# Kernel tuning notes

Measured on AMD Instinct MI355X. Metric: run time of the kernel, lower is better.

Reference implementation:

```python
import jax, jax.numpy as jnp
import numpy as np

KT = 0.5
KG = 0.5

def _ln(x, g, b, eps=1e-5):
    m = x.mean(-1, keepdims=True)
    v = ((x - m) ** 2).mean(-1, keepdims=True)
    return (x - m) / jnp.sqrt(v + eps) * g + b

def _sin_pe(pos, d):
    # pos: [...] float positions -> [..., d] sinusoidal encoding
    half = d // 2
    div = jnp.exp(jnp.arange(half, dtype=jnp.float32) * jnp.float32(-np.log(10000.0) * 2.0 / d))
    ang = pos[..., None].astype(jnp.float32) * div
    return jnp.concatenate([jnp.sin(ang), jnp.cos(ang)], axis=-1)

def _geo_encode(idx, emb_qk_w, w1, b1, w2, b2, ln1_g, ln1_b, ln2_g, ln2_b):
    gd = emb_qk_w.shape[-1]
    Lg = idx.shape[-1]
    x = emb_qk_w[idx]                                   # (B, S, Lg, gd)
    x = x + _sin_pe(jnp.arange(Lg, dtype=jnp.float32), gd)
    scale = 1.0 / np.sqrt(gd)
    for i in range(w1.shape[0]):
        s = jnp.einsum('bsqd,bskd->bsqk', x, x) * scale
        a = jax.nn.softmax(s, axis=-1)
        c = jnp.einsum('bsqk,bskd->bsqd', a, x)
        x = _ln(x + c, ln1_g[i], ln1_b[i])
        h = jax.nn.relu(x @ w1[i] + b1[i]) @ w2[i] + b2[i]
        x = _ln(x + h, ln2_g[i], ln2_b[i])
    return x.mean(-2)                                   # (B, S, gd)

def _forward(src_poi, src_quadkey, padding_mask, attn_mask, tgt_poi, tgt_quadkey,
             key_padding_mask, mem_mask, data_size,
             src_time, tm, gm, emb_poi_w, emb_qk_w,
             geo_ffn_w1, geo_ffn_b1, geo_ffn_w2, geo_ffn_b2,
             geo_ln1_g, geo_ln1_b, geo_ln2_g, geo_ln2_b,
             enc_wq, enc_wk, enc_wv, enc_ffn_w1, enc_ffn_b1, enc_ffn_w2, enc_ffn_b2,
             enc_ln1_g, enc_ln1_b, enc_ln2_g, enc_ln2_b,
             dec_wq, dec_wk, dec_wv, dec_ln_g, dec_ln_b, norm_g, norm_b):
    NEG = jnp.float32(-1e9)
    L = src_poi.shape[1]
    D = norm_g.shape[0]
    geo = lambda idx: _geo_encode(idx, emb_qk_w, geo_ffn_w1, geo_ffn_b1, geo_ffn_w2,
                                  geo_ffn_b2, geo_ln1_g, geo_ln1_b, geo_ln2_g, geo_ln2_b)
    src = jnp.concatenate([emb_poi_w[src_poi], geo(src_quadkey)], axis=-1)   # (B, L, D)
    tgt = jnp.concatenate([emb_poi_w[tgt_poi], geo(tgt_quadkey)], axis=-1)   # (B, Lt, D)
    # time-aware positional encoding: continuous positions from normalized timestamps
    t0 = src_time[:, :1]; tN = src_time[:, -1:]
    pos = (src_time - t0) / (tN - t0 + 1e-9) * (L - 1)
    src = src + _sin_pe(pos, D)
    # relation matrix: threshold intervals at kt/kg, then per-batch max-inversion (vectorizes the per-i loop)
    tmc = jnp.minimum(tm, KT)
    gmc = jnp.minimum(gm, KG)
    tmc = tmc.max(axis=(1, 2), keepdims=True) - tmc
    gmc = gmc.max(axis=(1, 2), keepdims=True) - gmc
    rel = tmc + gmc                                     # (B, L, L)
    scale = 1.0 / np.sqrt(D)
    emask = attn_mask[None, :, :] | padding_mask[:, None, :]
    for i in range(enc_wq.shape[0]):                    # Interval Aware Attention Blocks
        q = src @ enc_wq[i]; k = src @ enc_wk[i]; v = src @ enc_wv[i]
        s = jnp.einsum('bqd,bkd->bqk', q, k) * scale + rel
        a = jax.nn.softmax(jnp.where(emask, NEG, s), axis=-1)
        c = jnp.einsum('bqk,bkd->bqd', a, v)
        src = _ln(src + c, enc_ln1_g[i], enc_ln1_b[i])
        h = jax.nn.relu(src @ enc_ffn_w1[i] + enc_ffn_b1[i]) @ enc_ffn_w2[i] + enc_ffn_b2[i]
        src = _ln(src + h, enc_ln2_g[i], enc_ln2_b[i])
    # target-aware decoder (eval path: last encoder state broadcast over candidates)
    mem = jnp.broadcast_to(src[:, -1:, :], tgt.shape)
    dmask = mem_mask[None, :, :] | key_padding_mask[:, None, :]
    x = tgt
    for i in range(dec_wq.shape[0]):
        q = x @ dec_wq[i]; k = mem @ dec_wk[i]; v = mem @ dec_wv[i]
        s = jnp.einsum('bqd,bkd->bqk', q, k) * scale
        a = jax.nn.softmax(jnp.where(dmask, NEG, s), axis=-1)
        c = jnp.einsum('bqk,bkd->bqd', a, v)
        x = _ln(x + c, dec_ln_g[i], dec_ln_b[i])
    out = _ln(x + mem, norm_g, norm_b)
    return jnp.sum(out * tgt, axis=-1)                  # (B, Lt) matching scores

def setup_inputs():
    key = jax.random.key(0)
    ks = iter(jax.random.split(key, 64))
    nk = lambda: next(ks)
    B, L, Lg, Lt = 512, 100, 12, 101
    n_poi, n_qk = 100000, 4096
    ed, gd = 192, 64
    D = ed + gd
    Ng, Ni, Nd = 2, 2, 1
    p = lambda *s: (jax.random.normal(nk(), s, jnp.float32) * 0.02)
    return {
        'src_poi': jax.random.randint(nk(), (B, L), 0, n_poi),
        'src_quadkey': jax.random.randint(nk(), (B, L, Lg), 0, n_qk),
        'src_time': jnp.sort(jax.random.uniform(nk(), (B, L), jnp.float32) * 1e4, axis=-1),
        'tm': jax.random.uniform(nk(), (B, L, L), jnp.float32),
        'gm': jax.random.uniform(nk(), (B, L, L), jnp.float32),
        'padding_mask': jnp.zeros((B, L), bool),
        'attn_mask': jnp.triu(jnp.ones((L, L), bool), k=1),
        'tgt_poi': jax.random.randint(nk(), (B, Lt), 0, n_poi),
        'tgt_quadkey': jax.random.randint(nk(), (B, Lt, Lg), 0, n_qk),
        'key_padding_mask': jnp.zeros((B, Lt), bool),
        'mem_mask': jnp.zeros((Lt, Lt), bool),
        'data_size': jnp.full((B,), L, jnp.int32),
        'emb_poi_w': p(n_poi, ed),
        'emb_qk_w': p(n_qk, gd),
        'geo_ffn_w1': p(Ng, gd, 2 * gd), 'geo_ffn_b1': jnp.zeros((Ng, 2 * gd)),
        'geo_ffn_w2': p(Ng, 2 * gd, gd), 'geo_ffn_b2': jnp.zeros((Ng, gd)),
        'geo_ln1_g': jnp.ones((Ng, gd)), 'geo_ln1_b': jnp.zeros((Ng, gd)),
        'geo_ln2_g': jnp.ones((Ng, gd)), 'geo_ln2_b': jnp.zeros((Ng, gd)),
        'enc_wq': p(Ni, D, D), 'enc_wk': p(Ni, D, D), 'enc_wv': p(Ni, D, D),
        'enc_ffn_w1': p(Ni, D, 2 * D), 'enc_ffn_b1': jnp.zeros((Ni, 2 * D)),
        'enc_ffn_w2': p(Ni, 2 * D, D), 'enc_ffn_b2': jnp.zeros((Ni, D)),
        'enc_ln1_g': jnp.ones((Ni, D)), 'enc_ln1_b': jnp.zeros((Ni, D)),
        'enc_ln2_g': jnp.ones((Ni, D)), 'enc_ln2_b': jnp.zeros((Ni, D)),
        'dec_wq': p(Nd, D, D), 'dec_wk': p(Nd, D, D), 'dec_wv': p(Nd, D, D),
        'dec_ln_g': jnp.ones((Nd, D)), 'dec_ln_b': jnp.zeros((Nd, D)),
        'norm_g': jnp.ones((D,)), 'norm_b': jnp.zeros((D,)),
    }

def reference(src_poi, src_quadkey, src_time, tm, gm, padding_mask, attn_mask,
              tgt_poi, tgt_quadkey, key_padding_mask, mem_mask, data_size,
              emb_poi_w, emb_qk_w,
              geo_ffn_w1, geo_ffn_b1, geo_ffn_w2, geo_ffn_b2,
              geo_ln1_g, geo_ln1_b, geo_ln2_g, geo_ln2_b,
              enc_wq, enc_wk, enc_wv, enc_ffn_w1, enc_ffn_b1, enc_ffn_w2, enc_ffn_b2,
              enc_ln1_g, enc_ln1_b, enc_ln2_g, enc_ln2_b,
              dec_wq, dec_wk, dec_wv, dec_ln_g, dec_ln_b, norm_g, norm_b):
    return _forward(src_poi, src_quadkey, padding_mask, attn_mask, tgt_poi, tgt_quadkey,
                    key_padding_mask, mem_mask, data_size,
                    src_time, tm, gm, emb_poi_w, emb_qk_w,
                    geo_ffn_w1, geo_ffn_b1, geo_ffn_w2, geo_ffn_b2,
                    geo_ln1_g, geo_ln1_b, geo_ln2_g, geo_ln2_b,
                    enc_wq, enc_wk, enc_wv, enc_ffn_w1, enc_ffn_b1, enc_ffn_w2, enc_ffn_b2,
                    enc_ln1_g, enc_ln1_b, enc_ln2_g, enc_ln2_b,
                    dec_wq, dec_wk, dec_wv, dec_ln_g, dec_ln_b, norm_g, norm_b)
```

## Files before the change

kernel.cpp:

```cpp
#include <hip/hip_runtime.h>
#include <hip/hip_bf16.h>
#include <stdint.h>

typedef unsigned short u16;
typedef unsigned int   u32;
typedef __attribute__((ext_vector_type(8))) short v8s;
typedef __attribute__((ext_vector_type(4))) float v4f;

__device__ __forceinline__ float b2f(u16 u){ return __uint_as_float(((u32)u) << 16); }
__device__ __forceinline__ float lo2f(u32 u){ return __uint_as_float(u << 16); }
__device__ __forceinline__ float hi2f(u32 u){ return __uint_as_float(u & 0xffff0000u); }
__device__ __forceinline__ u16 f2b(float f){
    __hip_bfloat16 h = __float2bfloat16(f);
    return *reinterpret_cast<u16*>(&h);
}
__device__ __forceinline__ float ldm(const void* p, size_t i, int isbf){
    return isbf ? b2f(((const u16*)p)[i]) : ((const float*)p)[i];
}
__device__ __forceinline__ float wred_sum(float v){
    #pragma unroll
    for (int o = 32; o > 0; o >>= 1) v += __shfl_xor(v, o, 64);
    return v;
}
__device__ __forceinline__ float wred_max(float v){
    #pragma unroll
    for (int o = 32; o > 0; o >>= 1) v = fmaxf(v, __shfl_xor(v, o, 64));
    return v;
}
__device__ __forceinline__ float wred16_sum(float v){
    #pragma unroll
    for (int o = 8; o > 0; o >>= 1) v += __shfl_xor(v, o, 64);
    return v;
}
__device__ __forceinline__ float wred16_max(float v){
    #pragma unroll
    for (int o = 8; o > 0; o >>= 1) v = fmaxf(v, __shfl_xor(v, o, 64));
    return v;
}
__device__ __forceinline__ float block_sum256(float v, float* red, int tid){
    float s = wred_sum(v);
    __syncthreads();
    if ((tid & 63) == 0) red[tid >> 6] = s;
    __syncthreads();
    return red[0] + red[1] + red[2] + red[3];
}
__device__ __forceinline__ void block_sum2(float& a, float& b, float (*red)[2], int tid){
    a = wred_sum(a); b = wred_sum(b);
    __syncthreads();
    if ((tid & 63) == 0){ red[tid >> 6][0] = a; red[tid >> 6][1] = b; }
    __syncthreads();
    a = red[0][0] + red[1][0] + red[2][0] + red[3][0];
    b = red[0][1] + red[1][1] + red[2][1] + red[3][1];
}
__device__ __forceinline__ void lds_fence(){
    asm volatile("s_waitcnt lgkmcnt(0)" ::: "memory");
    __builtin_amdgcn_sched_barrier(0);
}

__global__ void probe_kernel(const u32* __restrict__ ng, int* __restrict__ flag){
    if (threadIdx.x == 0) *flag = (ng[0] == 0x3F803F80u) ? 1 : 0;
}

#define NSEG 25
struct ConvArgs {
    const void* src[NSEG];
    u16*        dst[NSEG];
    int         n[NSEG];
};
__global__ __launch_bounds__(256) void convert_kernel(ConvArgs a, const int* __restrict__ flag){
    int seg = blockIdx.y;
    int i = blockIdx.x * 256 + threadIdx.x;
    if (i >= a.n[seg]) return;
    int isbf = *flag;
    a.dst[seg][i] = f2b(ldm(a.src[seg], i, isbf));
}
__global__ __launch_bounds__(256) void convert_time_kernel(const void* __restrict__ src,
                                                           float* __restrict__ dst,
                                                           const int* __restrict__ flag){
    int i = blockIdx.x * 256 + threadIdx.x;
    if (i >= 51200) return;
    dst[i] = ldm(src, i, *flag);
}

__global__ __launch_bounds__(256) void packfrag_kernel(
    const u16* __restrict__ W, u16* __restrict__ out, int K, int N, int nlayer)
{
    int i = blockIdx.x * 256 + threadIdx.x;
    int total = nlayer * K * N;
    if (i >= total) return;
    int j = i & 7, lane = (i >> 3) & 63, fc = i >> 9;
    int CT = K >> 5, NT = N >> 4;
    int c = fc % CT, nt = (fc / CT) % NT, layer = fc / (CT * NT);
    int k = c * 32 + ((lane >> 4) << 3) + j, n = (nt << 4) + (lane & 15);
    out[i] = W[(layer * K + k) * N + n];
}

__global__ __launch_bounds__(256) void packfrag3_kernel(
    const u16* __restrict__ Wq, const u16* __restrict__ Wk, const u16* __restrict__ Wv,
    u16* __restrict__ out)
{
    int i = blockIdx.x * 256 + threadIdx.x;
    if (i >= 786432) return;
    int j = i & 7, lane = (i >> 3) & 63, fc = i >> 9;
    int c = fc & 7, nt = (fc >> 3) % 48, layer = fc / (8 * 48);
    int k = c * 32 + ((lane >> 4) << 3) + j, n = (nt << 4) + (lane & 15);
    const u16* W = (n < 256) ? Wq : (n < 512) ? Wk : Wv;
    out[i] = W[(layer * 256 + k) * 256 + (n & 255)];
}

template<int ACT, int SPLIT>
__global__ __launch_bounds__(256) void gemm2_kernel(
    const u16* __restrict__ A, const u16* __restrict__ Bf,
    const u16* __restrict__ bias,
    u16* __restrict__ C0, u16* __restrict__ C1, u16* __restrict__ C2,
    int M, int N, int K)
{
    const int tid = threadIdx.x, w = tid >> 6, lane = tid & 63;
    const int wm = w >> 1, wn = w & 1;
    const int m0 = blockIdx.x * 128 + wm * 64;
    const int n0 = blockIdx.y * 128 + wn * 64;
    const int CT = K >> 5;
    const int l15 = lane & 15, lg = lane >> 4;

    v4f acc[4][4];
    #pragma unroll
    for (int mt = 0; mt < 4; mt++)
        #pragma unroll
        for (int nt = 0; nt < 4; nt++) acc[mt][nt] = (v4f){0.f, 0.f, 0.f, 0.f};

    const u16* Arow = A + (size_t)(m0 + l15) * K + (lg << 3);
    const u16* Bbase = Bf + (((size_t)(n0 >> 4) * CT) << 9) + (lane << 3);

    for (int c = 0; c < CT; c++){
        v8s bfr[4];
        #pragma unroll
        for (int nt = 0; nt < 4; nt++)
            bfr[nt] = *(const v8s*)(Bbase + (((size_t)(nt * CT + c)) << 9));
        #pragma unroll
        for (int mt = 0; mt < 4; mt++){
            v8s af = *(const v8s*)(Arow + (size_t)(mt << 4) * K + (c << 5));
            #pragma unroll
            for (int nt = 0; nt < 4; nt++)
                acc[mt][nt] = __builtin_amdgcn_mfma_f32_16x16x32_bf16(af, bfr[nt], acc[mt][nt], 0, 0, 0);
        }
    }

    #pragma unroll
    for (int nt = 0; nt < 4; nt++){
        int colbase = n0 + (nt << 4);
        float bv = bias ? b2f(bias[colbase + l15]) : 0.f;
        u16* Cp; int cw;
        if (SPLIT){
            int nb = colbase >> 8;
            Cp = (nb == 0) ? C0 : (nb == 1) ? C1 : C2;
            cw = 256;
            colbase &= 255;
        } else { Cp = C0; cw = N; }
        #pragma unroll
        for (int mt = 0; mt < 4; mt++)
            #pragma unroll
            for (int r = 0; r < 4; r++){
                int row = m0 + (mt << 4) + (lg << 2) + r;
                float v = acc[mt][nt][r] + bv;
                if (ACT) v = fmaxf(v, 0.f);
                Cp[(size_t)row * cw + colbase + l15] = f2b(v);
            }
    }
}

__global__ __launch_bounds__(256) void gemm3_kernel(
    const u16* __restrict__ A, const u16* __restrict__ Bf,
    const u16* __restrict__ bias, u16* __restrict__ SRC,
    const u16* __restrict__ g, const u16* __restrict__ bta)
{
    __shared__ float red[64][4][2];
    const int tid = threadIdx.x, w = tid >> 6, lane = tid & 63;
    const int l15 = lane & 15, lg = lane >> 4;
    const int m0 = blockIdx.x * 64;
    const int n0 = w * 64;
    const int CT = 16;

    v4f acc[4][4];
    #pragma unroll
    for (int mt = 0; mt < 4; mt++)
        #pragma unroll
        for (int nt = 0; nt < 4; nt++) acc[mt][nt] = (v4f){0.f, 0.f, 0.f, 0.f};

    const u16* Arow = A + (size_t)(m0 + l15) * 512 + (lg << 3);
    const u16* Bbase = Bf + (((size_t)(n0 >> 4) * CT) << 9) + (lane << 3);

    for (int c = 0; c < CT; c++){
        v8s bfr[4];
        #pragma unroll
        for (int nt = 0; nt < 4; nt++)
            bfr[nt] = *(const v8s*)(Bbase + (((size_t)(nt * CT + c)) << 9));
        #pragma unroll
        for (int mt = 0; mt < 4; mt++){
            v8s af = *(const v8s*)(Arow + (size_t)(mt << 4) * 512 + (c << 5));
            #pragma unroll
            for (int nt = 0; nt < 4; nt++)
                acc[mt][nt] = __builtin_amdgcn_mfma_f32_16x16x32_bf16(af, bfr[nt], acc[mt][nt], 0, 0, 0);
        }
    }

    float bv[4];
    #pragma unroll
    for (int nt = 0; nt < 4; nt++) bv[nt] = b2f(bias[n0 + (nt << 4) + l15]);
    #pragma unroll
    for (int mt = 0; mt < 4; mt++){
        #pragma unroll
        for (int r = 0; r < 4; r++){
            int row = m0 + (mt << 4) + (lg << 2) + r;
            float s1 = 0.f, s2 = 0.f;
            #pragma unroll
            for (int nt = 0; nt < 4; nt++){
                int col = n0 + (nt << 4) + l15;
                float y = acc[mt][nt][r] + bv[nt] + b2f(SRC[(size_t)row * 256 + col]);
                acc[mt][nt][r] = y;
                s1 += y; s2 += y * y;
            }
            s1 = wred16_sum(s1); s2 = wred16_sum(s2);
            if (l15 == 0){
                int rr = (mt << 4) + (lg << 2) + r;
                red[rr][w][0] = s1; red[rr][w][1] = s2;
            }
        }
    }
    __syncthreads();
    float gv[4], bb[4];
    #pragma unroll
    for (int nt = 0; nt < 4; nt++){
        gv[nt] = b2f(g[n0 + (nt << 4) + l15]);
        bb[nt] = b2f(bta[n0 + (nt << 4) + l15]);
    }
    #pragma unroll
    for (int mt = 0; mt < 4; mt++){
        #pragma unroll
        for (int r = 0; r < 4; r++){
            int rr = (mt << 4) + (lg << 2) + r;
            int row = m0 + rr;
            float S1 = red[rr][0][0] + red[rr][1][0] + red[rr][2][0] + red[rr][3][0];
            float S2 = red[rr][0][1] + red[rr][1][1] + red[rr][2][1] + red[rr][3][1];
            float mu = S1 * (1.0f / 256.0f);
            float var = S2 * (1.0f / 256.0f) - mu * mu;
            float rs = rsqrtf(var + 1e-5f);
            #pragma unroll
            for (int nt = 0; nt < 4; nt++){
                int col = n0 + (nt << 4) + l15;
                SRC[(size_t)row * 256 + col] = f2b((acc[mt][nt][r] - mu) * rs * gv[nt] + bb[nt]);
            }
        }
    }
}

#define GX1(r,b) (((((r) << 7) | (b))) ^ (((r) & 7) << 4))
#define GH1(r,b) (((((r) << 8) | (b))) ^ (((r) & 7) << 4))

__global__ __launch_bounds__(64) void geo6_kernel(
    const int* __restrict__ src_qk, const int* __restrict__ tgt_qk,
    const u16* __restrict__ emb,
    const u16* __restrict__ w1f, const u16* __restrict__ b1,
    const u16* __restrict__ w2f, const u16* __restrict__ b2,
    const u16* __restrict__ ln1g, const u16* __restrict__ ln1b,
    const u16* __restrict__ ln2g, const u16* __restrict__ ln2b,
    u16* __restrict__ SRC, u16* __restrict__ TGT)
{
    __shared__ __align__(16) u16 xs[16 * 64];
    __shared__ __align__(16) u16 hs[16 * 128];
    __shared__ __align__(16) float Ps[16][20];

    int seq = blockIdx.x;
    const int* qk = src_qk;
    u16* outp = SRC;
    if (seq >= 51200){ qk = tgt_qk; outp = TGT; seq -= 51200; }

    const int lane = threadIdx.x;
    const int g = lane >> 4, m = lane & 15;

    v8s ones;
    #pragma unroll
    for (int j = 0; j < 8; j++) ones[j] = (short)0x3F80;

    {
        float dv = __expf(-(float)(lane & 31) * 0.28782313662425572f);
        const bool issin = lane < 32;
        #pragma unroll
        for (int t = 0; t < 12; t++){
            int idx = qk[seq * 12 + t];
            float ang = (float)t * dv;
            float pe = issin ? __sinf(ang) : __cosf(ang);
            xs[GX1(t, lane << 1) >> 1] = f2b(b2f(emb[idx * 64 + lane]) + pe);
        }
        #pragma unroll
        for (int r = 12; r < 16; r++) xs[GX1(r, lane << 1) >> 1] = (u16)0;
    }
    lds_fence();

    float fsum = 0.f;
    const bool isdiag = (g == (m >> 2)) && (m < 12);
    const int dr = m & 3;

    for (int layer = 0; layer < 2; layer++){
        v4f S = {0.f, 0.f, 0.f, 0.f};
        {
            v8s f0 = *(const v8s*)((const char*)xs + GX1(m, (g << 4)));
            v8s f1 = *(const v8s*)((const char*)xs + GX1(m, 64 + (g << 4)));
            S = __builtin_amdgcn_mfma_f32_16x16x32_bf16(f0, f0, S, 0, 0, 0);
            S = __builtin_amdgcn_mfma_f32_16x16x32_bf16(f1, f1, S, 0, 0, 0);
        }
        {
            float ex[4];
            #pragma unroll
            for (int r = 0; r < 4; r++) ex[r] = (m < 12) ? __expf(S[r] * 0.125f) : 0.f;
            #pragma unroll
            for (int r = 0; r < 4; r++){
                float s = wred16_sum(ex[r]);
                ex[r] = ex[r] / s;
            }
            #pragma unroll
            for (int r = 0; r < 4; r++) Ps[(g << 2) + r][m] = ex[r];
        }
        lds_fence();

        float y[12];
        {
            float xr[12];
            #pragma unroll
            for (int k = 0; k < 12; k++) xr[k] = b2f(xs[GX1(k, lane << 1) >> 1]);
            #pragma unroll
            for (int q = 0; q < 12; q++){
                float4 pa = *(const float4*)&Ps[q][0];
                float4 pb = *(const float4*)&Ps[q][4];
                float4 pc = *(const float4*)&Ps[q][8];
                float c = pa.x*xr[0]+pa.y*xr[1]+pa.z*xr[2]+pa.w*xr[3]
                        + pb.x*xr[4]+pb.y*xr[5]+pb.z*xr[6]+pb.w*xr[7]
                        + pc.x*xr[8]+pc.y*xr[9]+pc.z*xr[10]+pc.w*xr[11];
                y[q] = xr[q] + c;
                xs[GX1(q, lane << 1) >> 1] = f2b(y[q]);
            }
        }
        lds_fence();

        {
            v4f R = {0.f,0.f,0.f,0.f}, Q = {0.f,0.f,0.f,0.f};
            v8s f0 = *(const v8s*)((const char*)xs + GX1(m, (g << 4)));
            v8s f1 = *(const v8s*)((const char*)xs + GX1(m, 64 + (g << 4)));
            R = __builtin_amdgcn_mfma_f32_16x16x32_bf16(f0, ones, R, 0, 0, 0);
            R = __builtin_amdgcn_mfma_f32_16x16x32_bf16(f1, ones, R, 0, 0, 0);
            Q = __builtin_amdgcn_mfma_f32_16x16x32_bf16(f0, f0, Q, 0, 0, 0);
            Q = __builtin_amdgcn_mfma_f32_16x16x32_bf16(f1, f1, Q, 0, 0, 0);
            if (isdiag){ Ps[m][16] = R[dr]; Ps[m][17] = Q[dr]; }
        }
        lds_fence();
        {
            float g1 = b2f(ln1g[layer * 64 + lane]), bb1 = b2f(ln1b[layer * 64 + lane]);
            #pragma unroll
            for (int q = 0; q < 12; q++){
                float2 st = *(const float2*)&Ps[q][16];
                float mu = st.x * 0.015625f;
                float var = st.y * 0.015625f - mu * mu;
                xs[GX1(q, lane << 1) >> 1] = f2b((y[q] - mu) * rsqrtf(var + 1e-5f) * g1 + bb1);
            }
        }
        lds_fence();

        {
            v8s a0 = *(const v8s*)((const char*)xs + GX1(m, (g << 4)));
            v8s a1 = *(const v8s*)((const char*)xs + GX1(m, 64 + (g << 4)));
            const u16* wf1 = w1f + layer * 8192;
            #pragma unroll
            for (int nt = 0; nt < 8; nt++){
                v8s bfa = *(const v8s*)(wf1 + (((nt << 1) + 0) << 9) + (lane << 3));
                v8s bfb = *(const v8s*)(wf1 + (((nt << 1) + 1) << 9) + (lane << 3));
                v4f h = {0.f, 0.f, 0.f, 0.f};
                h = __builtin_amdgcn_mfma_f32_16x16x32_bf16(a0, bfa, h, 0, 0, 0);
                h = __builtin_amdgcn_mfma_f32_16x16x32_bf16(a1, bfb, h, 0, 0, 0);
                float bia = b2f(b1[layer * 128 + (nt << 4) + m]);
                #pragma unroll
                for (int r = 0; r < 4; r++)
                    hs[GH1((g << 2) + r, ((nt << 4) | m) << 1) >> 1] = f2b(fmaxf(h[r] + bia, 0.f));
            }
        }
        lds_fence();

        {
            v8s ha[4];
            #pragma unroll
            for (int c = 0; c < 4; c++)
                ha[c] = *(const v8s*)((const char*)hs + GH1(m, (c << 6) + (g << 4)));
            lds_fence();
            float* os = (float*)hs;
            const u16* wf2 = w2f + layer * 8192;
            #pragma unroll
            for (int nt = 0; nt < 4; nt++){
                v4f o = {0.f, 0.f, 0.f, 0.f};
                #pragma unroll
                for (int c = 0; c < 4; c++){
                    v8s bf = *(const v8s*)(wf2 + ((((nt << 2) + c) << 9) + (lane << 3)));
                    o = __builtin_amdgcn_mfma_f32_16x16x32_bf16(ha[c], bf, o, 0, 0, 0);
                }
                float bo = b2f(b2[layer * 64 + (nt << 4) + m]);
                #pragma unroll
                for (int r = 0; r < 4; r++)
                    os[((g << 2) + r) * 64 + (nt << 4) + m] = o[r] + bo;
            }
        }
        lds_fence();

        {
            const float* os = (const float*)hs;
            #pragma unroll
            for (int q = 0; q < 12; q++){
                y[q] = b2f(xs[GX1(q, lane << 1) >> 1]) + os[q * 64 + lane];
            }
            lds_fence();
            #pragma unroll
            for (int q = 0; q < 12; q++)
                xs[GX1(q, lane << 1) >> 1] = f2b(y[q]);
        }
        lds_fence();
        {
            v4f R = {0.f,0.f,0.f,0.f}, Q = {0.f,0.f,0.f,0.f};
            v8s f0 = *(const v8s*)((const char*)xs + GX1(m, (g << 4)));
            v8s f1 = *(const v8s*)((const char*)xs + GX1(m, 64 + (g << 4)));
            R = __builtin_amdgcn_mfma_f32_16x16x32_bf16(f0, ones, R, 0, 0, 0);
            R = __builtin_amdgcn_mfma_f32_16x16x32_bf16(f1, ones, R, 0, 0, 0);
            Q = __builtin_amdgcn_mfma_f32_16x16x32_bf16(f0, f0, Q, 0, 0, 0);
            Q = __builtin_amdgcn_mfma_f32_16x16x32_bf16(f1, f1, Q, 0, 0, 0);
            if (isdiag){ Ps[m][16] = R[dr]; Ps[m][17] = Q[dr]; }
        }
        lds_fence();
        {
            float g2 = b2f(ln2g[layer * 64 + lane]), bb2 = b2f(ln2b[layer * 64 + lane]);
            #pragma unroll
            for (int q = 0; q < 12; q++){
                float2 st = *(const float2*)&Ps[q][16];
                float mu = st.x * 0.015625f;
                float var = st.y * 0.015625f - mu * mu;
                float xv = (y[q] - mu) * rsqrtf(var + 1e-5f) * g2 + bb2;
                if (layer == 0) xs[GX1(q, lane << 1) >> 1] = f2b(xv);
                else            fsum += xv;
            }
        }
        lds_fence();
    }
    outp[(size_t)seq * 256 + 192 + lane] = f2b(fsum * (1.0f / 12.0f));
}

__global__ __launch_bounds__(256) void embed_src_kernel(
    const int* __restrict__ poi, const float* __restrict__ timev,
    const void* __restrict__ emb_poi, u16* __restrict__ src,
    const int* __restrict__ flag)
{
    const int bl = blockIdx.x;
    const int d  = threadIdx.x;
    const int b  = bl / 100;
    const int isbf = *flag;
    float t0 = timev[b * 100];
    float tN = timev[b * 100 + 99];
    float tv = timev[bl];
    float pos = (tv - t0) / (tN - t0 + 1e-9f) * 99.0f;
    int j = d & 127;
    float dvv = __expf(-(float)j * 0.07195578415606393f);
    float ang = pos * dvv;
    float pe = (d < 128) ? __sinf(ang) : __cosf(ang);
    size_t off = (size_t)bl * 256 + d;
    float val = (d < 192) ? ldm(emb_poi, (size_t)poi[bl] * 192 + d, isbf) : b2f(src[off]);
    src[off] = f2b(val + pe);
}

__global__ __launch_bounds__(256) void embed_tgt_kernel(
    const int* __restrict__ poi, const void* __restrict__ emb_poi,
    u16* __restrict__ tgt, int n, const int* __restrict__ flag)
{
    int i = blockIdx.x * 256 + threadIdx.x;
    if (i >= n * 192) return;
    int bt = i / 192; int d = i - bt * 192;
    tgt[(size_t)bt * 256 + d] = f2b(ldm(emb_poi, (size_t)poi[bt] * 192 + d, *flag));
}

__global__ __launch_bounds__(256) void relmax_kernel(
    const void* __restrict__ tm, const void* __restrict__ gm,
    float* __restrict__ relm, const int* __restrict__ flag)
{
    const int b = blockIdx.x, tid = threadIdx.x;
    const int isbf = *flag;
    size_t base = (size_t)b * 10000;
    float tmax = -1e30f, gmax = -1e30f;
    for (int i = tid; i < 10000; i += 256){
        tmax = fmaxf(tmax, fminf(ldm(tm, base + i, isbf), 0.5f));
        gmax = fmaxf(gmax, fminf(ldm(gm, base + i, isbf), 0.5f));
    }
    tmax = wred_max(tmax); gmax = wred_max(gmax);
    __shared__ float st[4], sg[4];
    if ((tid & 63) == 0){ st[tid >> 6] = tmax; sg[tid >> 6] = gmax; }
    __syncthreads();
    if (tid == 0){
        relm[b * 2]     = fmaxf(fmaxf(st[0], st[1]), fmaxf(st[2], st[3]));
        relm[b * 2 + 1] = fmaxf(fmaxf(sg[0], sg[1]), fmaxf(sg[2], sg[3]));
    }
}

__global__ __launch_bounds__(256) void attn_kernel(
    const u16* __restrict__ QB, const u16* __restrict__ Kg, const u16* __restrict__ Vg,
    u16* __restrict__ SRC,
    const void* __restrict__ tmp_, const void* __restrict__ gmp_,
    const float* __restrict__ relm,
    const u16* __restrict__ lng, const u16* __restrict__ lnb,
    const int* __restrict__ flag)
{
    __shared__ __align__(16) u16 KV[100][264];
    __shared__ __align__(16) u16 Amat[50][112];

    const int blk = blockIdx.x;
    const int b = blk >> 1, h = blk & 1;
    const int tid = threadIdx.x;
    const int w = tid >> 6, lane = tid & 63;
    const int l15 = lane & 15, lg = lane >> 4;
    const int q0 = h * 50;
    const int nk = q0 + 50;
    const int isbf = *flag;
    const float tmax = relm[b * 2], gmax = relm[b * 2 + 1];

    const u16* Vb = Vg + (size_t)b * 100 * 256;
    for (int i = tid; i < nk * 128; i += 256){
        int row = i >> 7, c2 = (i & 127) * 2;
        *(ushort2*)&KV[row][c2] = *(const ushort2*)(Vb + row * 256 + c2);
    }

    const int ntc = (h == 0) ? 4 : 7;
    const int qrow = q0 + w * 16 + l15;
    const u16* Aq = QB + ((size_t)b * 100 + (qrow < 100 ? qrow : 99)) * 256 + (lg << 3);
    const u16* Kb = Kg + (size_t)b * 100 * 256;
    v4f S[7];
    #pragma unroll
    for (int nt = 0; nt < 7; nt++) S[nt] = (v4f){0.f, 0.f, 0.f, 0.f};
    const u16* Bp[7];
    for (int nt = 0; nt < ntc; nt++){
        int kt = nt * 16 + l15;
        Bp[nt] = Kb + (size_t)(kt < 100 ? kt : 99) * 256 + (lg << 3);
    }
    for (int c = 0; c < 8; c++){
        v8s af = *(const v8s*)(Aq + (c << 5));
        for (int nt = 0; nt < ntc; nt++){
            v8s bf = *(const v8s*)(Bp[nt] + (c << 5));
            S[nt] = __builtin_amdgcn_mfma_f32_16x16x32_bf16(af, bf, S[nt], 0, 0, 0);
        }
    }

    float P[7][4];
    #pragma unroll
    for (int r = 0; r < 4; r++){
        int qrel = w * 16 + (lg << 2) + r;
        int q = q0 + qrel;
        int qc = q < 100 ? q : 99;
        size_t rbase = ((size_t)b * 100 + qc) * 100;
        float sv[7];
        float mx = -1e30f;
        for (int nt = 0; nt < ntc; nt++){
            int kt = nt * 16 + l15;
            int ktc = kt < 100 ? kt : 99;
            float rel = (tmax - fminf(ldm(tmp_, rbase + ktc, isbf), 0.5f))
                      + (gmax - fminf(ldm(gmp_, rbase + ktc, isbf), 0.5f));
            float s = S[nt][r] * 0.0625f + rel;
            if (kt > q) s = -1e30f;
            sv[nt] = s;
            mx = fmaxf(mx, s);
        }
        mx = wred16_max(mx);
        float sum = 0.f;
        for (int nt = 0; nt < ntc; nt++){ sv[nt] = __expf(sv[nt] - mx); sum += sv[nt]; }
        sum = wred16_sum(sum);
        float inv = 1.0f / sum;
        for (int nt = 0; nt < ntc; nt++) P[nt][r] = sv[nt] * inv;
    }
    #pragma unroll
    for (int r = 0; r < 4; r++){
        int qrel = w * 16 + (lg << 2) + r;
        if (qrel < 50){
            for (int nt = 0; nt < ntc; nt++)
                Amat[qrel][nt * 16 + l15] = f2b(P[nt][r]);
        }
    }
    __syncthreads();

    for (int qq = 0; qq < 13; qq++){
        const int qr = qq * 4 + w;
        const int q  = q0 + qr;
        if (qr < 50){
            float o00 = 0.f, o01 = 0.f, o10 = 0.f, o11 = 0.f;
            const int kfull = (q + 1) & ~7;
            for (int k8 = 0; k8 < (kfull >> 3); k8++){
                uint4 av = *(const uint4*)&Amat[qr][k8 * 8];
                float p[8] = { lo2f(av.x), hi2f(av.x), lo2f(av.y), hi2f(av.y),
                               lo2f(av.z), hi2f(av.z), lo2f(av.w), hi2f(av.w) };
                #pragma unroll
                for (int j = 0; j < 8; j++){
                    int k = k8 * 8 + j;
                    u32 v0 = *(const u32*)&KV[k][2 * lane];
                    u32 v1 = *(const u32*)&KV[k][128 + 2 * lane];
                    o00 += p[j] * lo2f(v0); o01 += p[j] * hi2f(v0);
                    o10 += p[j] * lo2f(v1); o11 += p[j] * hi2f(v1);
                }
            }
            for (int k = kfull; k <= q; k++){
                float a = b2f(Amat[qr][k]);
                u32 v0 = *(const u32*)&KV[k][2 * lane];
                u32 v1 = *(const u32*)&KV[k][128 + 2 * lane];
                o00 += a * lo2f(v0); o01 += a * hi2f(v0);
                o10 += a * lo2f(v1); o11 += a * hi2f(v1);
            }
            u16* Sg = SRC + ((size_t)b * 100 + q) * 256;
            u32 s0v = *(const u32*)&Sg[2 * lane];
            u32 s1v = *(const u32*)&Sg[128 + 2 * lane];
            float y0 = o00 + lo2f(s0v), y1 = o01 + hi2f(s0v);
            float y2 = o10 + lo2f(s1v), y3 = o11 + hi2f(s1v);
            float s1 = y0 + y1 + y2 + y3;
            float s2 = y0*y0 + y1*y1 + y2*y2 + y3*y3;
            s1 = wred_sum(s1); s2 = wred_sum(s2);
            float mu = s1 * (1.0f / 256.0f);
            float var = s2 * (1.0f / 256.0f) - mu * mu;
            float rs = rsqrtf(var + 1e-5f);
            u32 g0 = *(const u32*)&lng[2 * lane], g1 = *(const u32*)&lng[128 + 2 * lane];
            u32 b0 = *(const u32*)&lnb[2 * lane], b1 = *(const u32*)&lnb[128 + 2 * lane];
            ushort2 w0, w1;
            w0.x = f2b((y0 - mu) * rs * lo2f(g0) + lo2f(b0));
            w0.y = f2b((y1 - mu) * rs * hi2f(g0) + hi2f(b0));
            w1.x = f2b((y2 - mu) * rs * lo2f(g1) + lo2f(b1));
            w1.y = f2b((y3 - mu) * rs * hi2f(g1) + hi2f(b1));
            *(ushort2*)&Sg[2 * lane]       = w0;
            *(ushort2*)&Sg[128 + 2 * lane] = w1;
        }
    }
}

__global__ __launch_bounds__(256) void decv_kernel(
    const u16* __restrict__ SRC, const u16* __restrict__ wv, float* __restrict__ VS)
{
    __shared__ float sv[256];
    const int b = blockIdx.x, n = threadIdx.x;
    const u16* s = SRC + ((size_t)b * 100 + 99) * 256;
    sv[n] = b2f(s[n]);
    __syncthreads();
    float acc = 0.f;
    for (int d = 0; d < 256; d++) acc += sv[d] * b2f(wv[d * 256 + n]);
    VS[(size_t)b * 256 + n] = acc;
}

__global__ __launch_bounds__(256) void decfinal_kernel(
    const u16* __restrict__ TGT, const u16* __restrict__ SRC,
    const float* __restrict__ VS,
    const u16* __restrict__ dlg, const u16* __restrict__ dlb,
    const u16* __restrict__ ng,  const u16* __restrict__ nb,
    void* __restrict__ outp, const int* __restrict__ flag)
{
    __shared__ float red2[4][2];
    __shared__ float red1[4];
    const int bt = blockIdx.x, d = threadIdx.x;
    const int b = bt / 101;
    float tg  = b2f(TGT[(size_t)bt * 256 + d]);
    float mem = b2f(SRC[((size_t)b * 100 + 99) * 256 + d]);
    float y = tg + VS[(size_t)b * 256 + d];
    float a = y, bb = y * y;
    block_sum2(a, bb, red2, d);
    float mu1 = a * (1.0f / 256.0f);
    float v1 = bb * (1.0f / 256.0f) - mu1 * mu1;
    float x = (y - mu1) * rsqrtf(v1 + 1e-5f) * b2f(dlg[d]) + b2f(dlb[d]);
    float y2 = x + mem;
    float a2 = y2, b2_ = y2 * y2;
    block_sum2(a2, b2_, red2, d);
    float mu2 = a2 * (1.0f / 256.0f);
    float v2 = b2_ * (1.0f / 256.0f) - mu2 * mu2;
    float o = (y2 - mu2) * rsqrtf(v2 + 1e-5f) * b2f(ng[d]) + b2f(nb[d]);
    float tot = block_sum256(o * tg, red1, d);
    if (d == 0){
        if (*flag) ((u16*)outp)[bt] = f2b(tot);
        else       ((float*)outp)[bt] = tot;
    }
}

extern "C" void kernel_launch(void* const* d_in, const int* in_sizes, int n_in,
                              void* d_out, int out_size, void* d_ws, size_t ws_size,
                              hipStream_t stream)
{
    char* ws = (char*)d_ws;
    size_t off = 0;
    auto AL = [&](size_t bytes){ size_t o = off; off += (bytes + 255) & ~(size_t)255; return o; };
    const size_t FLAGO = AL(4);
    const size_t CTIME = AL(51200 * 4);
    const size_t CEQK  = AL(262144 * 2);
    const size_t CGW1  = AL(16384 * 2), CGB1 = AL(256 * 2), CGW2 = AL(16384 * 2), CGB2 = AL(128 * 2);
    const size_t CGL1G = AL(128 * 2), CGL1B = AL(128 * 2), CGL2G = AL(128 * 2), CGL2B = AL(128 * 2);
    const size_t CEWQ  = AL(131072 * 2), CEWK = AL(131072 * 2), CEWV = AL(131072 * 2);
    const size_t CEW1  = AL(262144 * 2), CEB1 = AL(1024 * 2), CEW2 = AL(262144 * 2), CEB2 = AL(512 * 2);
    const size_t CEL1G = AL(512 * 2), CEL1B = AL(512 * 2), CEL2G = AL(512 * 2), CEL2B = AL(512 * 2);
    const size_t CDWV  = AL(65536 * 2), CDLG = AL(256 * 2), CDLB = AL(256 * 2), CNG = AL(256 * 2), CNB = AL(256 * 2);
    const size_t W1FO  = AL(16384 * 2), W2FO = AL(16384 * 2);
    const size_t QKVFO = AL(786432 * 2);
    const size_t W1FEO = AL(524288 * 2);
    const size_t W2FEO = AL(524288 * 2);
    const size_t RELMO = AL(512 * 2 * 4);
    const size_t VSO   = AL(512 * 256 * 4);
    const size_t SRCO  = AL((size_t)51200 * 256 * 2);
    const size_t TGTO  = AL((size_t)51712 * 256 * 2);
    const size_t B1O   = AL((size_t)51200 * 256 * 2);
    const size_t B2O   = AL((size_t)51200 * 256 * 2);
    const size_t B3O   = AL((size_t)51200 * 256 * 2);
    (void)ws_size; (void)in_sizes; (void)n_in; (void)out_size;

    int*   FLAG = (int*)(ws + FLAGO);
    float* CT   = (float*)(ws + CTIME);
    u16 *cEQK=(u16*)(ws+CEQK), *cGW1=(u16*)(ws+CGW1), *cGB1=(u16*)(ws+CGB1), *cGW2=(u16*)(ws+CGW2),
        *cGB2=(u16*)(ws+CGB2), *cGL1G=(u16*)(ws+CGL1G), *cGL1B=(u16*)(ws+CGL1B), *cGL2G=(u16*)(ws+CGL2G),
        *cGL2B=(u16*)(ws+CGL2B), *cEWQ=(u16*)(ws+CEWQ), *cEWK=(u16*)(ws+CEWK), *cEWV=(u16*)(ws+CEWV),
        *cEW1=(u16*)(ws+CEW1), *cEB1=(u16*)(ws+CEB1), *cEW2=(u16*)(ws+CEW2), *cEB2=(u16*)(ws+CEB2),
        *cEL1G=(u16*)(ws+CEL1G), *cEL1B=(u16*)(ws+CEL1B), *cEL2G=(u16*)(ws+CEL2G), *cEL2B=(u16*)(ws+CEL2B),
        *cDWV=(u16*)(ws+CDWV), *cDLG=(u16*)(ws+CDLG), *cDLB=(u16*)(ws+CDLB), *cNG=(u16*)(ws+CNG),
        *cNB=(u16*)(ws+CNB);
    u16* W1F   = (u16*)(ws + W1FO);
    u16* W2F   = (u16*)(ws + W2FO);
    u16* QKVF  = (u16*)(ws + QKVFO);
    u16* W1FE  = (u16*)(ws + W1FEO);
    u16* W2FE  = (u16*)(ws + W2FEO);
    float* RELM = (float*)(ws + RELMO);
    float* VS   = (float*)(ws + VSO);
    u16* SRC = (u16*)(ws + SRCO);
    u16* TGT = (u16*)(ws + TGTO);
    u16* B1  = (u16*)(ws + B1O);
    u16* B2  = (u16*)(ws + B2O);
    u16* B3  = (u16*)(ws + B3O);
    u16* Hh  = B2;

    const int* src_poi = (const int*)d_in[0];
    const int* src_qk  = (const int*)d_in[1];
    const int* tgt_poi = (const int*)d_in[7];
    const int* tgt_qk  = (const int*)d_in[8];

    probe_kernel<<<1, 64, 0, stream>>>((const u32*)d_in[38], FLAG);

    ConvArgs ca;
    const int srcidx[NSEG] = {13,14,15,16,17,18,19,20,21,22,23,24,25,26,27,28,29,30,31,32,35,36,37,38,39};
    u16* dsts[NSEG] = {cEQK,cGW1,cGB1,cGW2,cGB2,cGL1G,cGL1B,cGL2G,cGL2B,cEWQ,cEWK,cEWV,
                       cEW1,cEB1,cEW2,cEB2,cEL1G,cEL1B,cEL2G,cEL2B,cDWV,cDLG,cDLB,cNG,cNB};
    const int ns[NSEG] = {262144,16384,256,16384,128,128,128,128,128,131072,131072,131072,
                          262144,1024,262144,512,512,512,512,512,65536,256,256,256,256};
    for (int i = 0; i < NSEG; i++){ ca.src[i] = d_in[srcidx[i]]; ca.dst[i] = dsts[i]; ca.n[i] = ns[i]; }
    convert_kernel<<<dim3(1024, NSEG), 256, 0, stream>>>(ca, FLAG);
    convert_time_kernel<<<200, 256, 0, stream>>>(d_in[2], CT, FLAG);

    packfrag_kernel<<<64, 256, 0, stream>>>(cGW1, W1F, 64, 128, 2);
    packfrag_kernel<<<64, 256, 0, stream>>>(cGW2, W2F, 128, 64, 2);
    packfrag3_kernel<<<3072, 256, 0, stream>>>(cEWQ, cEWK, cEWV, QKVF);
    packfrag_kernel<<<1024, 256, 0, stream>>>(cEW1, W1FE, 256, 512, 2);
    packfrag_kernel<<<1024, 256, 0, stream>>>(cEW2, W2FE, 512, 256, 2);

    geo6_kernel<<<102912, 64, 0, stream>>>(src_qk, tgt_qk, cEQK, W1F, cGB1, W2F, cGB2,
                                           cGL1G, cGL1B, cGL2G, cGL2B, SRC, TGT);
    embed_src_kernel<<<51200, 256, 0, stream>>>(src_poi, CT, d_in[12], SRC, FLAG);
    embed_tgt_kernel<<<(51712 * 192 + 255) / 256, 256, 0, stream>>>(tgt_poi, d_in[12], TGT, 51712, FLAG);
    relmax_kernel<<<512, 256, 0, stream>>>(d_in[3], d_in[4], RELM, FLAG);

    for (int i = 0; i < 2; i++){
        gemm2_kernel<0,1><<<dim3(400, 6), 256, 0, stream>>>(SRC, QKVF + (size_t)i * 196608, nullptr,
                                                            B1, B2, B3, 51200, 768, 256);
        attn_kernel<<<1024, 256, 0, stream>>>(B1, B2, B3, SRC, d_in[3], d_in[4], RELM,
                                              cEL1G + i * 256, cEL1B + i * 256, FLAG);
        gemm2_kernel<1,0><<<dim3(400, 4), 256, 0, stream>>>(SRC, W1FE + (size_t)i * 131072, cEB1 + i * 512,
                                                            Hh, nullptr, nullptr, 51200, 512, 256);
        gemm3_kernel<<<800, 256, 0, stream>>>(Hh, W2FE + (size_t)i * 131072, cEB2 + i * 256,
                                              SRC, cEL2G + i * 256, cEL2B + i * 256);
    }

    decv_kernel<<<512, 256, 0, stream>>>(SRC, cDWV, VS);
    decfinal_kernel<<<51712, 256, 0, stream>>>(TGT, SRC, VS, cDLG, cDLB, cNG, cNB, d_out, FLAG);
}
```

Measured before the change: 1.262 ms.

## Fuse embedding kernels into geo encoder and move attention-value product to MFMA

Merges the POI embedding lookup and time-aware positional encoding into the geo encoder kernel, removing two separate launches and a read-modify-write pass over SRC/TGT. Inside the geo encoder, the attention-weighted sum becomes an MFMA on a bf16 probability tile times a transposed copy of x, replacing per-lane scalar FMAs. Intermediate data is kept in MFMA-fragment layout so the residual and layernorm steps run on registers, and the final mean over positions uses shuffles. It also swaps the bf16 conversion for a hand-written round-to-nearest-even bit trick. The trade-offs are extra LDS writes for the transposed x and bf16 rounding of the attention probabilities.

After: 1.419 ms. 12.5% more time.

```diff
diff --git a/kernel.cpp b/kernel.cpp
--- a/kernel.cpp
+++ b/kernel.cpp
@@ -11,8 +11,9 @@
 __device__ __forceinline__ float lo2f(u32 u){ return __uint_as_float(u << 16); }
 __device__ __forceinline__ float hi2f(u32 u){ return __uint_as_float(u & 0xffff0000u); }
 __device__ __forceinline__ u16 f2b(float f){
-    __hip_bfloat16 h = __float2bfloat16(f);
-    return *reinterpret_cast<u16*>(&h);
+    u32 x = __float_as_uint(f);
+    u32 r = (x + 0x7fffu + ((x >> 16) & 1u)) >> 16;
+    return (u16)r;
 }
 __device__ __forceinline__ float ldm(const void* p, size_t i, int isbf){
     return isbf ? b2f(((const u16*)p)[i]) : ((const float*)p)[i];
@@ -256,31 +257,41 @@
 #define GX1(r,b) (((((r) << 7) | (b))) ^ (((r) & 7) << 4))
 #define GH1(r,b) (((((r) << 8) | (b))) ^ (((r) & 7) << 4))
 
-__global__ __launch_bounds__(64) void geo6_kernel(
+__global__ __launch_bounds__(64) void geo7_kernel(
     const int* __restrict__ src_qk, const int* __restrict__ tgt_qk,
+    const int* __restrict__ src_poi, const int* __restrict__ tgt_poi,
+    const void* __restrict__ emb_poi, const float* __restrict__ CTm,
     const u16* __restrict__ emb,
     const u16* __restrict__ w1f, const u16* __restrict__ b1,
     const u16* __restrict__ w2f, const u16* __restrict__ b2,
     const u16* __restrict__ ln1g, const u16* __restrict__ ln1b,
     const u16* __restrict__ ln2g, const u16* __restrict__ ln2b,
-    u16* __restrict__ SRC, u16* __restrict__ TGT)
+    u16* __restrict__ SRC, u16* __restrict__ TGT, const int* __restrict__ flag)
 {
     __shared__ __align__(16) u16 xs[16 * 64];
-    __shared__ __align__(16) u16 hs[16 * 128];
-    __shared__ __align__(16) float Ps[16][20];
+    __shared__ __align__(16) u16 uni[2560];
+    __shared__ __align__(16) u16 PA[16 * 40];
+    __shared__ __align__(16) float st[16][2];
 
     int seq = blockIdx.x;
-    const int* qk = src_qk;
-    u16* outp = SRC;
-    if (seq >= 51200){ qk = tgt_qk; outp = TGT; seq -= 51200; }
+    const int* qk; const int* poi; u16* outp; bool is_src;
+    if (seq < 51200){ qk = src_qk; poi = src_poi; outp = SRC; is_src = true; }
+    else            { seq -= 51200; qk = tgt_qk; poi = tgt_poi; outp = TGT; is_src = false; }
 
     const int lane = threadIdx.x;
     const int g = lane >> 4, m = lane & 15;
+    const int isbf = *flag;
 
     v8s ones;
     #pragma unroll
     for (int j = 0; j < 8; j++) ones[j] = (short)0x3F80;
 
+    u16* xT = uni;
+
+    for (int i = lane; i < 320; i += 64){
+        int r = i / 20, c = 12 + (i % 20);
+        PA[r * 40 + c] = 0;
+    }
     {
         float dv = __expf(-(float)(lane & 31) * 0.28782313662425572f);
         const bool issin = lane < 32;
@@ -289,134 +300,60 @@
             int idx = qk[seq * 12 + t];
             float ang = (float)t * dv;
             float pe = issin ? __sinf(ang) : __cosf(ang);
-            xs[GX1(t, lane << 1) >> 1] = f2b(b2f(emb[idx * 64 + lane]) + pe);
+            u16 bv = f2b(b2f(emb[idx * 64 + lane]) + pe);
+            xs[GX1(t, lane << 1) >> 1] = bv;
+            xT[lane * 40 + t] = bv;
         }
         #pragma unroll
         for (int r = 12; r < 16; r++) xs[GX1(r, lane << 1) >> 1] = (u16)0;
+        #pragma unroll
+        for (int k = 12; k < 32; k++) xT[lane * 40 + k] = (u16)0;
     }
     lds_fence();
 
-    float fsum = 0.f;
-    const bool isdiag = (g == (m >> 2)) && (m < 12);
-    const int dr = m & 3;
+    float fs = 0.f;
 
     for (int layer = 0; layer < 2; layer++){
-        v4f S = {0.f, 0.f, 0.f, 0.f};
         {
+            v4f S = {0.f, 0.f, 0.f, 0.f};
             v8s f0 = *(const v8s*)((const char*)xs + GX1(m, (g << 4)));
             v8s f1 = *(const v8s*)((const char*)xs + GX1(m, 64 + (g << 4)));
             S = __builtin_amdgcn_mfma_f32_16x16x32_bf16(f0, f0, S, 0, 0, 0);
             S = __builtin_amdgcn_mfma_f32_16x16x32_bf16(f1, f1, S, 0, 0, 0);
-        }
-        {
             float ex[4];
             #pragma unroll
             for (int r = 0; r < 4; r++) ex[r] = (m < 12) ? __expf(S[r] * 0.125f) : 0.f;
             #pragma unroll
             for (int r = 0; r < 4; r++){
                 float s = wred16_sum(ex[r]);
-                ex[r] = ex[r] / s;
-            }
-            #pragma unroll
-            for (int r = 0; r < 4; r++) Ps[(g << 2) + r][m] = ex[r];
+                PA[((g << 2) + r) * 40 + m] = f2b(ex[r] / s);
+            }
         }
         lds_fence();
 
-        float y[12];
+        float y[4][4];
         {
-            float xr[12];
-            #pragma unroll
-            for (int k = 0; k < 12; k++) xr[k] = b2f(xs[GX1(k, lane << 1) >> 1]);
-            #pragma unroll
-            for (int q = 0; q < 12; q++){
-                float4 pa = *(const float4*)&Ps[q][0];
-                float4 pb = *(const float4*)&Ps[q][4];
-                float4 pc = *(const float4*)&Ps[q][8];
-                float c = pa.x*xr[0]+pa.y*xr[1]+pa.z*xr[2]+pa.w*xr[3]
-                        + pb.x*xr[4]+pb.y*xr[5]+pb.z*xr[6]+pb.w*xr[7]
-                        + pc.x*xr[8]+pc.y*xr[9]+pc.z*xr[10]+pc.w*xr[11];
-                y[q] = xr[q] + c;
-                xs[GX1(q, lane << 1) >> 1] = f2b(y[q]);
-            }
-        }
-        lds_fence();
-
-        {
-            v4f R = {0.f,0.f,0.f,0.f}, Q = {0.f,0.f,0.f,0.f};
-            v8s f0 = *(const v8s*)((const char*)xs + GX1(m, (g << 4)));
-            v8s f1 = *(const v8s*)((const char*)xs + GX1(m, 64 + (g << 4)));
-            R = __builtin_amdgcn_mfma_f32_16x16x32_bf16(f0, ones, R, 0, 0, 0);
-            R = __builtin_amdgcn_mfma_f32_16x16x32_bf16(f1, ones, R, 0, 0, 0);
-            Q = __builtin_amdgcn_mfma_f32_16x16x32_bf16(f0, f0, Q, 0, 0, 0);
-            Q = __builtin_amdgcn_mfma_f32_16x16x32_bf16(f1, f1, Q, 0, 0, 0);
-            if (isdiag){ Ps[m][16] = R[dr]; Ps[m][17] = Q[dr]; }
-        }
-        lds_fence();
-        {
-            float g1 = b2f(ln1g[layer * 64 + lane]), bb1 = b2f(ln1b[layer * 64 + lane]);
-            #pragma unroll
-            for (int q = 0; q < 12; q++){
-                float2 st = *(const float2*)&Ps[q][16];
-                float mu = st.x * 0.015625f;
-                float var = st.y * 0.015625f - mu * mu;
-                xs[GX1(q, lane << 1) >> 1] = f2b((y[q] - mu) * rsqrtf(var + 1e-5f) * g1 + bb1);
-            }
-        }
-        lds_fence();
-
-        {
-            v8s a0 = *(const v8s*)((const char*)xs + GX1(m, (g << 4)));
-            v8s a1 = *(const v8s*)((const char*)xs + GX1(m, 64 + (g << 4)));
-            const u16* wf1 = w1f + layer * 8192;
-            #pragma unroll
-            for (int nt = 0; nt < 8; nt++){
-                v8s bfa = *(const v8s*)(wf1 + (((nt << 1) + 0) << 9) + (lane << 3));
-                v8s bfb = *(const v8s*)(wf1 + (((nt << 1) + 1) << 9) + (lane << 3));
-                v4f h = {0.f, 0.f, 0.f, 0.f};
-                h = __builtin_amdgcn_mfma_f32_16x16x32_bf16(a0, bfa, h, 0, 0, 0);
-                h = __builtin_amdgcn_mfma_f32_16x16x32_bf16(a1, bfb, h, 0, 0, 0);
-                float bia = b2f(b1[layer * 128 + (nt << 4) + m]);
-                #pragma unroll
-                for (int r = 0; r < 4; r++)
-                    hs[GH1((g << 2) + r, ((nt << 4) | m) << 1) >> 1] = f2b(fmaxf(h[r] + bia, 0.f));
-            }
-        }
-        lds_fence();
-
-        {
-            v8s ha[4];
-            #pragma unroll
-            for (int c = 0; c < 4; c++)
-                ha[c] = *(const v8s*)((const char*)hs + GH1(m, (c << 6) + (g << 4)));
-            lds_fence();
-            float* os = (float*)hs;
-            const u16* wf2 = w2f + layer * 8192;
+            v8s pa = *(const v8s*)(PA + m * 40 + (g << 3));
+            v4f C[4];
             #pragma unroll
             for (int nt = 0; nt < 4; nt++){
-                v4f o = {0.f, 0.f, 0.f, 0.f};
-                #pragma unroll
-                for (int c = 0; c < 4; c++){
-                    v8s bf = *(const v8s*)(wf2 + ((((nt << 2) + c) << 9) + (lane << 3)));
-                    o = __builtin_amdgcn_mfma_f32_16x16x32_bf16(ha[c], bf, o, 0, 0, 0);
+                v8s bfx = *(const v8s*)(xT + ((nt << 4) + m) * 40 + (g << 3));
+                C[nt] = __builtin_amdgcn_mfma_f32_16x16x32_bf16(pa, bfx, (v4f){0.f,0.f,0.f,0.f}, 0, 0, 0);
+            }
+            #pragma unroll
+            for (int nt = 0; nt < 4; nt++)
+                #pragma unroll
+                for (int r = 0; r < 4; r++){
+                    int row = (g << 2) + r, col = (nt << 4) + m;
+                    y[nt][r] = C[nt][r] + b2f(xs[GX1(row, col << 1) >> 1]);
                 }
-                float bo = b2f(b2[layer * 64 + (nt << 4) + m]);
-                #pragma unroll
-                for (int r = 0; r < 4; r++)
-                    os[((g << 2) + r) * 64 + (nt << 4) + m] = o[r] + bo;
-            }
-        }
-        lds_fence();
-
-        {
-            const float* os = (const float*)hs;
-            #pragma unroll
-            for (int q = 0; q < 12; q++){
-                y[q] = b2f(xs[GX1(q, lane << 1) >> 1]) + os[q * 64 + lane];
-            }
-            lds_fence();
-            #pragma unroll
-            for (int q = 0; q < 12; q++)
-                xs[GX1(q, lane << 1) >> 1] = f2b(y[q]);
+            #pragma unroll
+            for (int nt = 0; nt < 4; nt++)
+                #pragma unroll
+                for (int r = 0; r < 4; r++){
+                    int row = (g << 2) + r, col = (nt << 4) + m;
+                    xs[GX1(row, col << 1) >> 1] = f2b(y[nt][r]);
+                }
         }
         lds_fence();
         {
@@ -427,56 +364,154 @@
             R = __builtin_amdgcn_mfma_f32_16x16x32_bf16(f1, ones, R, 0, 0, 0);
             Q = __builtin_amdgcn_mfma_f32_16x16x32_bf16(f0, f0, Q, 0, 0, 0);
             Q = __builtin_amdgcn_mfma_f32_16x16x32_bf16(f1, f1, Q, 0, 0, 0);
-            if (isdiag){ Ps[m][16] = R[dr]; Ps[m][17] = Q[dr]; }
+            if (g == (m >> 2)){ st[m][0] = R[m & 3]; st[m][1] = Q[m & 3]; }
         }
         lds_fence();
         {
-            float g2 = b2f(ln2g[layer * 64 + lane]), bb2 = b2f(ln2b[layer * 64 + lane]);
-            #pragma unroll
-            for (int q = 0; q < 12; q++){
-                float2 st = *(const float2*)&Ps[q][16];
-                float mu = st.x * 0.015625f;
-                float var = st.y * 0.015625f - mu * mu;
-                float xv = (y[q] - mu) * rsqrtf(var + 1e-5f) * g2 + bb2;
-                if (layer == 0) xs[GX1(q, lane << 1) >> 1] = f2b(xv);
-                else            fsum += xv;
+            #pragma unroll
+            for (int nt = 0; nt < 4; nt++){
+                float g1 = b2f(ln1g[layer * 64 + (nt << 4) + m]);
+                float bb1 = b2f(ln1b[layer * 64 + (nt << 4) + m]);
+                #pragma unroll
+                for (int r = 0; r < 4; r++){
+                    int row = (g << 2) + r, col = (nt << 4) + m;
+                    float mu = st[row][0] * 0.015625f;
+                    float var = st[row][1] * 0.015625f - mu * mu;
+                    xs[GX1(row, col << 1) >> 1] = f2b((y[nt][r] - mu) * rsqrtf(var + 1e-5f) * g1 + bb1);
+                }
             }
         }
         lds_fence();
-    }
-    outp[(size_t)seq * 256 + 192 + lane] = f2b(fsum * (1.0f / 12.0f));
-}
-
-__global__ __launch_bounds__(256) void embed_src_kernel(
-    const int* __restrict__ poi, const float* __restrict__ timev,
-    const void* __restrict__ emb_poi, u16* __restrict__ src,
-    const int* __restrict__ flag)
-{
-    const int bl = blockIdx.x;
-    const int d  = threadIdx.x;
-    const int b  = bl / 100;
-    const int isbf = *flag;
-    float t0 = timev[b * 100];
-    float tN = timev[b * 100 + 99];
-    float tv = timev[bl];
-    float pos = (tv - t0) / (tN - t0 + 1e-9f) * 99.0f;
-    int j = d & 127;
-    float dvv = __expf(-(float)j * 0.07195578415606393f);
-    float ang = pos * dvv;
-    float pe = (d < 128) ? __sinf(ang) : __cosf(ang);
-    size_t off = (size_t)bl * 256 + d;
-    float val = (d < 192) ? ldm(emb_poi, (size_t)poi[bl] * 192 + d, isbf) : b2f(src[off]);
-    src[off] = f2b(val + pe);
-}
-
-__global__ __launch_bounds__(256) void embed_tgt_kernel(
-    const int* __restrict__ poi, const void* __restrict__ emb_poi,
-    u16* __restrict__ tgt, int n, const int* __restrict__ flag)
-{
-    int i = blockIdx.x * 256 + threadIdx.x;
-    if (i >= n * 192) return;
-    int bt = i / 192; int d = i - bt * 192;
-    tgt[(size_t)bt * 256 + d] = f2b(ldm(emb_poi, (size_t)poi[bt] * 192 + d, *flag));
+
+        {
+            u16* hs = uni;
+            v8s a0 = *(const v8s*)((const char*)xs + GX1(m, (g << 4)));
+            v8s a1 = *(const v8s*)((const char*)xs + GX1(m, 64 + (g << 4)));
+            const u16* wf1 = w1f + layer * 8192;
+            #pragma unroll
+            for (int nt = 0; nt < 8; nt++){
+                v8s bfa = *(const v8s*)(wf1 + (((nt << 1) + 0) << 9) + (lane << 3));
+                v8s bfb = *(const v8s*)(wf1 + (((nt << 1) + 1) << 9) + (lane << 3));
+                v4f h = {0.f, 0.f, 0.f, 0.f};
+                h = __builtin_amdgcn_mfma_f32_16x16x32_bf16(a0, bfa, h, 0, 0, 0);
+                h = __builtin_amdgcn_mfma_f32_16x16x32_bf16(a1, bfb, h, 0, 0, 0);
+                float bia = b2f(b1[layer * 128 + (nt << 4) + m]);
+                #pragma unroll
+                for (int r = 0; r < 4; r++)
+                    hs[GH1((g << 2) + r, (((nt << 4) | m) << 1)) >> 1] = f2b(fmaxf(h[r] + bia, 0.f));
+            }
+        }
+        lds_fence();
+
+        {
+            const u16* hs = uni;
+            v8s ha[4];
+            #pragma unroll
+            for (int c = 0; c < 4; c++)
+                ha[c] = *(const v8s*)((const char*)hs + GH1(m, (c << 6) + (g << 4)));
+            lds_fence();
+            const u16* wf2 = w2f + layer * 8192;
+            #pragma unroll
+            for (int nt = 0; nt < 4; nt++){
+                v4f o = {0.f, 0.f, 0.f, 0.f};
+                #pragma unroll
+                for (int c = 0; c < 4; c++){
+                    v8s bf = *(const v8s*)(wf2 + ((((nt << 2) + c) << 9) + (lane << 3)));
+                    o = __builtin_amdgcn_mfma_f32_16x16x32_bf16(ha[c], bf, o, 0, 0, 0);
+                }
+                float bo = b2f(b2[layer * 64 + (nt << 4) + m]);
+                #pragma unroll
+                for (int r = 0; r < 4; r++){
+                    int row = (g << 2) + r, col = (nt << 4) + m;
+                    y[nt][r] = o[nt != nt ? 0 : r] + bo + b2f(xs[GX1(row, col << 1) >> 1]);
+                }
+            }
+            #pragma unroll
+            for (int nt = 0; nt < 4; nt++)
+                #pragma unroll
+                for (int r = 0; r < 4; r++){
+                    int row = (g << 2) + r, col = (nt << 4) + m;
+                    xs[GX1(row, col << 1) >> 1] = f2b(y[nt][r]);
+                }
+        }
+        lds_fence();
+        {
+            v4f R = {0.f,0.f,0.f,0.f}, Q = {0.f,0.f,0.f,0.f};
+            v8s f0 = *(const v8s*)((const char*)xs + GX1(m, (g << 4)));
+            v8s f1 = *(const v8s*)((const char*)xs + GX1(m, 64 + (g << 4)));
+            R = __builtin_amdgcn_mfma_f32_16x16x32_bf16(f0, ones, R, 0, 0, 0);
+            R = __builtin_amdgcn_mfma_f32_16x16x32_bf16(f1, ones, R, 0, 0, 0);
+            Q = __builtin_amdgcn_mfma_f32_16x16x32_bf16(f0, f0, Q, 0, 0, 0);
+            Q = __builtin_amdgcn_mfma_f32_16x16x32_bf16(f1, f1, Q, 0, 0, 0);
+            if (g == (m >> 2)){ st[m][0] = R[m & 3]; st[m][1] = Q[m & 3]; }
+        }
+        lds_fence();
+        {
+            float xv[4][4];
+            #pragma unroll
+            for (int nt = 0; nt < 4; nt++){
+                float g2 = b2f(ln2g[layer * 64 + (nt << 4) + m]);
+                float bb2 = b2f(ln2b[layer * 64 + (nt << 4) + m]);
+                #pragma unroll
+                for (int r = 0; r < 4; r++){
+                    int row = (g << 2) + r;
+                    float mu = st[row][0] * 0.015625f;
+                    float var = st[row][1] * 0.015625f - mu * mu;
+                    xv[nt][r] = (y[nt][r] - mu) * rsqrtf(var + 1e-5f) * g2 + bb2;
+                }
+            }
+            if (layer == 0){
+                #pragma unroll
+                for (int nt = 0; nt < 4; nt++)
+                    #pragma unroll
+                    for (int r = 0; r < 4; r++){
+                        int row = (g << 2) + r, col = (nt << 4) + m;
+                        u16 bv = f2b(xv[nt][r]);
+                        xs[GX1(row, col << 1) >> 1] = bv;
+                        xT[col * 40 + row] = bv;
+                    }
+            } else {
+                float tot[4];
+                #pragma unroll
+                for (int nt = 0; nt < 4; nt++){
+                    float p = 0.f;
+                    if (g < 3){
+                        #pragma unroll
+                        for (int r = 0; r < 4; r++) p += xv[nt][r];
+                    }
+                    p += __shfl_xor(p, 16, 64);
+                    p += __shfl_xor(p, 32, 64);
+                    tot[nt] = p;
+                }
+                fs = (g == 0) ? tot[0] : (g == 1) ? tot[1] : (g == 2) ? tot[2] : tot[3];
+            }
+        }
+        lds_fence();
+    }
+
+    const float geo_out = fs * (1.0f / 12.0f);
+    const int pidx = poi[seq];
+    u16* row = outp + (size_t)seq * 256;
+    float e0 = ldm(emb_poi, (size_t)pidx * 192 + lane, isbf);
+    float e1 = ldm(emb_poi, (size_t)pidx * 192 + 64 + lane, isbf);
+    float e2 = ldm(emb_poi, (size_t)pidx * 192 + 128 + lane, isbf);
+    if (is_src){
+        int b = seq / 100;
+        float t0 = CTm[b * 100], tN = CTm[b * 100 + 99], tv = CTm[seq];
+        float pos = (tv - t0) / (tN - t0 + 1e-9f) * 99.0f;
+        float dv0 = __expf(-(float)lane * 0.07195578415606393f);
+        float dv1 = __expf(-(float)(lane + 64) * 0.07195578415606393f);
+        float a0 = pos * dv0, a1 = pos * dv1;
+        row[lane]        = f2b(e0 + __sinf(a0));
+        row[lane + 64]   = f2b(e1 + __sinf(a1));
+        row[lane + 128]  = f2b(e2 + __cosf(a0));
+        row[lane + 192]  = f2b(geo_out + __cosf(a1));
+    } else {
+        row[lane]        = f2b(e0);
+        row[lane + 64]   = f2b(e1);
+        row[lane + 128]  = f2b(e2);
+        row[lane + 192]  = f2b(geo_out);
+    }
 }
 
 __global__ __launch_bounds__(256) void relmax_kernel(
@@ -754,10 +789,9 @@
     packfrag_kernel<<<1024, 256, 0, stream>>>(cEW1, W1FE, 256, 512, 2);
     packfrag_kernel<<<1024, 256, 0, stream>>>(cEW2, W2FE, 512, 256, 2);
 
-    geo6_kernel<<<102912, 64, 0, stream>>>(src_qk, tgt_qk, cEQK, W1F, cGB1, W2F, cGB2,
-                                           cGL1G, cGL1B, cGL2G, cGL2B, SRC, TGT);
-    embed_src_kernel<<<51200, 256, 0, stream>>>(src_poi, CT, d_in[12], SRC, FLAG);
-    embed_tgt_kernel<<<(51712 * 192 + 255) / 256, 256, 0, stream>>>(tgt_poi, d_in[12], TGT, 51712, FLAG);
+    geo7_kernel<<<102912, 64, 0, stream>>>(src_qk, tgt_qk, src_poi, tgt_poi,
+                                           d_in[12], CT, cEQK, W1F, cGB1, W2F, cGB2,
+                                           cGL1G, cGL1B, cGL2G, cGL2B, SRC, TGT, FLAG);
     relmax_kernel<<<512, 256, 0, stream>>>(d_in[3], d_in[4], RELM, FLAG);
 
     for (int i = 0; i < 2; i++){
```
